# Performance work log

Measured on AMD Instinct MI355X. Metric: run time of the kernel, lower is better.

The kernel has to match this reference:

```python
import jax, jax.numpy as jnp
import numpy as np

TOP_K = 2


def setup_inputs() -> dict:
    key = jax.random.key(0)
    ks = jax.random.split(key, 5)
    B, S, H, E, I = 2, 1024, 1024, 16, 1024
    scale = 1.0 / np.sqrt(H)
    return {
        "hidden_states": jax.random.normal(ks[0], (B, S, H), dtype=jnp.float32),
        "router_w": jax.random.normal(ks[1], (E, H), dtype=jnp.float32) * scale,   # nn.Linear(H,E).weight
        "gate_w": jax.random.normal(ks[2], (E, I, H), dtype=jnp.float32) * scale,  # per-expert Linear(H,I).weight
        "up_w": jax.random.normal(ks[3], (E, I, H), dtype=jnp.float32) * scale,
        "down_w": jax.random.normal(ks[4], (E, H, I), dtype=jnp.float32) * (1.0 / np.sqrt(I)),
    }


def reference(hidden_states, router_w, gate_w, up_w, down_w):
    orig_shape = hidden_states.shape
    x = hidden_states.reshape(-1, orig_shape[-1])  # [T, H]
    T = x.shape[0]
    E = router_w.shape[0]

    # Router: sigmoid -> top-k -> normalize
    logits = jnp.einsum("th,eh->te", x, router_w)           # [T, E]
    scores = jax.nn.sigmoid(logits)
    weights, indices = jax.lax.top_k(scores, TOP_K)         # [T, K]
    weights = weights / (weights.sum(axis=-1, keepdims=True) + 1e-20)

    # Dense per-token-per-expert combine weight (0 for unrouted pairs) ==
    # exact math of the torch gather/index_add loop.
    w_full = jnp.zeros((T, E), dtype=x.dtype).at[
        jnp.arange(T)[:, None], indices
    ].add(weights)                                          # [T, E]

    # Expert MLPs (SwiGLU) computed for all experts, zero-weighted combine.
    g = jax.nn.silu(jnp.einsum("th,eih->tei", x, gate_w))   # [T, E, I]
    u = jnp.einsum("th,eih->tei", x, up_w)                  # [T, E, I]
    out = jnp.einsum("te,tei,ehi->th", w_full, g * u, down_w)  # [T, H]
    return out.reshape(orig_shape)
```

## Files before the change

### kernel.cpp

```cpp
#include <hip/hip_runtime.h>
#include <stdint.h>

#define T_TOK 2048
#define H_DIM 1024
#define E_NUM 16
#define I_DIM 1024
#define TOTAL_ROWS (2 * T_TOK)
#define CPAD 16

typedef short bf16x8 __attribute__((ext_vector_type(8)));
typedef float f32x4 __attribute__((ext_vector_type(4)));

__device__ __forceinline__ void async_copy16(const void* g, void* l) {
  __builtin_amdgcn_global_load_lds(
      (const __attribute__((address_space(1))) void*)g,
      (__attribute__((address_space(3))) void*)l, 16, 0, 0);
}

__device__ __forceinline__ uint32_t f2bf(float f) {
  uint32_t u = __float_as_uint(f);
  return (u + 0x7FFFu + ((u >> 16) & 1u)) >> 16;
}
__device__ __forceinline__ uint32_t pk2bf(float lo, float hi) {
  return f2bf(lo) | (f2bf(hi) << 16);
}

#define WS_COUNTS 0
#define WS_OFFSETS 2048
#define WS_TOKENS 4096
#define WS_WTS (4096 + 131072)
#define WS_XBF (4096 + 262144)
#define WS_HBUF (WS_XBF + 4194304)
#define WS_GBUF (WS_HBUF + 8388608)
#define WS_UBUF (WS_GBUF + 33554432)
#define WS_DBUF (WS_UBUF + 33554432)
#define WS_NEED (WS_DBUF + 33554432)

__global__ __launch_bounds__(256) void router_prep_kernel(
    const float* __restrict__ x, const float* __restrict__ rw,
    const float* __restrict__ gate, const float* __restrict__ up,
    const float* __restrict__ down, uint16_t* __restrict__ xbf,
    int* __restrict__ counts, int* __restrict__ tokens,
    float* __restrict__ wts, uint16_t* __restrict__ gbuf,
    uint16_t* __restrict__ ubuf, uint16_t* __restrict__ dbuf) {
  const int bid = blockIdx.x;
  const int tid = threadIdx.x;

  if (bid < 512) {
    const int t = bid * 4 + (tid >> 6);
    const int lane = tid & 63;

    float4 xv[4];
    float acc[E_NUM];
#pragma unroll
    for (int e = 0; e < E_NUM; ++e) acc[e] = 0.f;

#pragma unroll
    for (int rep = 0; rep < 4; ++rep) {
      const int h0 = rep * 256 + lane * 4;
      xv[rep] = *(const float4*)(x + (size_t)t * H_DIM + h0);
      uint2 p;
      p.x = pk2bf(xv[rep].x, xv[rep].y);
      p.y = pk2bf(xv[rep].z, xv[rep].w);
      *(uint2*)(xbf + (size_t)t * H_DIM + h0) = p;
    }

#pragma unroll
    for (int e = 0; e < E_NUM; ++e) {
#pragma unroll
      for (int rep = 0; rep < 4; ++rep) {
        const float4 rv =
            *(const float4*)(rw + (size_t)e * H_DIM + rep * 256 + lane * 4);
        acc[e] += xv[rep].x * rv.x + xv[rep].y * rv.y + xv[rep].z * rv.z +
                  xv[rep].w * rv.w;
      }
    }

#pragma unroll
    for (int e = 0; e < E_NUM; ++e) {
      float v = acc[e];
#pragma unroll
      for (int off = 32; off > 0; off >>= 1) v += __shfl_xor(v, off);
      acc[e] = v;
    }

    if (lane < 2) {
      float s[E_NUM];
#pragma unroll
      for (int e = 0; e < E_NUM; ++e) s[e] = 1.f / (1.f + expf(-acc[e]));
      int i1 = 0;
      float v1 = s[0];
#pragma unroll
      for (int e = 1; e < E_NUM; ++e)
        if (s[e] > v1) { v1 = s[e]; i1 = e; }
      int i2 = -1;
      float v2 = -1.f;
#pragma unroll
      for (int e = 0; e < E_NUM; ++e)
        if (e != i1 && s[e] > v2) { v2 = s[e]; i2 = e; }
      const float inv = 1.f / (v1 + v2 + 1e-20f);
      const int pe = (lane == 0) ? i1 : i2;
      const float pw = ((lane == 0) ? v1 : v2) * inv;
      const int slot = atomicAdd(&counts[pe * CPAD], 1);
      tokens[pe * T_TOK + slot] = t;
      wts[pe * T_TOK + slot] = pw;
    }
    return;
  }

  const int tt = bid - 512;
  const int mat = tt >> 12;
  const int r = tt & 4095;
  const int e = r >> 8;
  const int nt = (r >> 4) & 15;
  const int kt = r & 15;
  const float* W = (mat == 0) ? gate : (mat == 1) ? up : down;
  uint16_t* D = (mat == 0) ? gbuf : (mat == 1) ? ubuf : dbuf;
  const float* src = W + ((size_t)e * 1024 + (size_t)nt * 64) * 1024 + kt * 64;
  uint16_t* dst = D + ((size_t)((e * 16 + nt) * 16 + kt)) * 4096;

#pragma unroll
  for (int h = 0; h < 2; ++h) {
    const int c = tid + h * 256;
    const int m = c >> 3;
    const int kq = (c & 7) ^ (m & 7);
    const float* s = src + (size_t)m * 1024 + kq * 8;
    const float4 a = *(const float4*)s;
    const float4 b = *(const float4*)(s + 4);
    uint4 p;
    p.x = pk2bf(a.x, a.y);
    p.y = pk2bf(a.z, a.w);
    p.z = pk2bf(b.x, b.y);
    p.w = pk2bf(b.z, b.w);
    *(uint4*)(dst + (size_t)c * 8) = p;
  }
}

__global__ void offsets_kernel(const int* __restrict__ counts,
                               int* __restrict__ offsets) {
  if (threadIdx.x == 0) {
    int a = 0;
    for (int e = 0; e < E_NUM; ++e) {
      offsets[e] = a;
      a += counts[e * CPAD];
    }
    offsets[E_NUM] = a;
  }
}

__global__ __launch_bounds__(256, 2) void gemm1_kernel(
    const uint16_t* __restrict__ xbf, const uint16_t* __restrict__ gbuf,
    const uint16_t* __restrict__ ubuf, const int* __restrict__ counts,
    const int* __restrict__ offsets, const int* __restrict__ tokens,
    const float* __restrict__ wts, uint16_t* __restrict__ hbuf) {
  const int e = blockIdx.z;
  const int count = counts[e * CPAD];
  const int m0 = blockIdx.y * 128;
  if (m0 >= count) return;
  const int n0t = blockIdx.x;

  __shared__ __align__(16) uint16_t As[2][128 * 64];
  __shared__ __align__(16) uint16_t Bgs[2][64 * 64];
  __shared__ __align__(16) uint16_t Bus[2][64 * 64];
  __shared__ int tok_s[128];
  __shared__ float wt_s[128];

  const int tid = threadIdx.x;
  if (tid < 128) {
    const int slot = m0 + tid;
    int tk = 0;
    float w = 0.f;
    if (slot < count) {
      tk = tokens[e * T_TOK + slot];
      w = wts[e * T_TOK + slot];
    }
    tok_s[tid] = tk;
    wt_s[tid] = w;
  }
  __syncthreads();

  const uint16_t* a_g[4];
  int a_c[4];
#pragma unroll
  for (int j = 0; j < 4; ++j) {
    const int c = j * 256 + tid;
    const int m = c >> 3;
    const int kq = (c & 7) ^ (m & 7);
    a_g[j] = xbf + (size_t)tok_s[m] * H_DIM + kq * 8;
    a_c[j] = c * 8;
  }
  const uint16_t* g_g = gbuf + (size_t)((e * 16 + n0t) * 16) * 4096;
  const uint16_t* u_g = ubuf + (size_t)((e * 16 + n0t) * 16) * 4096;
  const int bc0 = tid * 8, bc1 = (tid + 256) * 8;

  const int wave = tid >> 6, lane = tid & 63;
  const int wm = wave * 32;
  const int lc = lane & 15, lq = lane >> 4;
  const int l7 = lc & 7;

  f32x4 accg[2][4], accu[2][4];
  const f32x4 zero4 = {0.f, 0.f, 0.f, 0.f};
#pragma unroll
  for (int i = 0; i < 2; ++i)
#pragma unroll
    for (int j = 0; j < 4; ++j) {
      accg[i][j] = zero4;
      accu[i][j] = zero4;
    }

  int am[2], bn[4];
#pragma unroll
  for (int i = 0; i < 2; ++i) am[i] = (wm + i * 16 + lc) * 64;
#pragma unroll
  for (int i = 0; i < 4; ++i) bn[i] = (i * 16 + lc) * 64;

#pragma unroll
  for (int j = 0; j < 4; ++j) async_copy16(a_g[j], &As[0][a_c[j]]);
  async_copy16(g_g + bc0, &Bgs[0][bc0]);
  async_copy16(g_g + bc1, &Bgs[0][bc1]);
  async_copy16(u_g + bc0, &Bus[0][bc0]);
  async_copy16(u_g + bc1, &Bus[0][bc1]);
  __syncthreads();

  int cur = 0;
  for (int kt = 0; kt < 16; ++kt) {
    const bool more = (kt < 15);
    if (more) {
      const int ko = (kt + 1) * 64;
      const int bo = (kt + 1) * 4096;
      const int nb = cur ^ 1;
#pragma unroll
      for (int j = 0; j < 4; ++j) async_copy16(a_g[j] + ko, &As[nb][a_c[j]]);
      async_copy16(g_g + bo + bc0, &Bgs[nb][bc0]);
      async_copy16(g_g + bo + bc1, &Bgs[nb][bc1]);
      async_copy16(u_g + bo + bc0, &Bus[nb][bc0]);
      async_copy16(u_g + bo + bc1, &Bus[nb][bc1]);
    }

#pragma unroll
    for (int ks = 0; ks < 2; ++ks) {
      const int kswz = ((ks * 4 + lq) ^ l7) * 8;
      bf16x8 af[2], bg[4], bu[4];
#pragma unroll
      for (int i = 0; i < 2; ++i)
        af[i] = *(const bf16x8*)&As[cur][am[i] + kswz];
#pragma unroll
      for (int i = 0; i < 4; ++i) {
        bg[i] = *(const bf16x8*)&Bgs[cur][bn[i] + kswz];
        bu[i] = *(const bf16x8*)&Bus[cur][bn[i] + kswz];
      }
#pragma unroll
      for (int im = 0; im < 2; ++im)
#pragma unroll
        for (int in = 0; in < 4; ++in) {
          accg[im][in] = __builtin_amdgcn_mfma_f32_16x16x32_bf16(
              af[im], bg[in], accg[im][in], 0, 0, 0);
          accu[im][in] = __builtin_amdgcn_mfma_f32_16x16x32_bf16(
              af[im], bu[in], accu[im][in], 0, 0, 0);
        }
    }

    if (more) {
      __syncthreads();
      cur ^= 1;
    }
  }

  const int off_e = offsets[e];
#pragma unroll
  for (int im = 0; im < 2; ++im) {
#pragma unroll
    for (int r = 0; r < 4; ++r) {
      const int row = wm + im * 16 + lq * 4 + r;
      const int slot = m0 + row;
      if (slot < count) {
        const float w = wt_s[row];
        uint16_t* hrow = hbuf + (size_t)(off_e + slot) * I_DIM + n0t * 64;
#pragma unroll
        for (int in = 0; in < 4; ++in) {
          const float g = accg[im][in][r];
          const float u = accu[im][in][r];
          const float hv = g / (1.f + __expf(-g)) * u * w;
          hrow[in * 16 + lc] = (uint16_t)f2bf(hv);
        }
      }
    }
  }
}

__global__ __launch_bounds__(256, 3) void gemm2_kernel(
    const uint16_t* __restrict__ hbuf, const uint16_t* __restrict__ dbuf,
    const int* __restrict__ counts, const int* __restrict__ offsets,
    const int* __restrict__ tokens, float* __restrict__ out) {
  const int e = blockIdx.z;
  const int count = counts[e * CPAD];
  const int m0 = blockIdx.y * 128;
  if (m0 >= count) return;
  const int n0t = blockIdx.x;

  __shared__ __align__(16) uint16_t As[2][128 * 64];
  __shared__ __align__(16) uint16_t Bs[2][64 * 64];
  __shared__ int tok_s[128];

  const int tid = threadIdx.x;
  const int off_e = offsets[e];
  if (tid < 128) {
    const int slot = m0 + tid;
    tok_s[tid] = (slot < count) ? tokens[e * T_TOK + slot] : 0;
  }

  const uint16_t* a_g[4];
  int a_c[4];
#pragma unroll
  for (int j = 0; j < 4; ++j) {
    const int c = j * 256 + tid;
    const int m = c >> 3;
    const int kq = (c & 7) ^ (m & 7);
    int r = off_e + m0 + m;
    if (r > TOTAL_ROWS - 1) r = TOTAL_ROWS - 1;
    a_g[j] = hbuf + (size_t)r * I_DIM + kq * 8;
    a_c[j] = c * 8;
  }
  const uint16_t* d_g = dbuf + (size_t)((e * 16 + n0t) * 16) * 4096;
  const int bc0 = tid * 8, bc1 = (tid + 256) * 8;

  const int wave = tid >> 6, lane = tid & 63;
  const int wm = wave * 32;
  const int lc = lane & 15, lq = lane >> 4;
  const int l7 = lc & 7;

  f32x4 acc[2][4];
  const f32x4 zero4 = {0.f, 0.f, 0.f, 0.f};
#pragma unroll
  for (int i = 0; i < 2; ++i)
#pragma unroll
    for (int j = 0; j < 4; ++j) acc[i][j] = zero4;

  int am[2], bn[4];
#pragma unroll
  for (int i = 0; i < 2; ++i) am[i] = (wm + i * 16 + lc) * 64;
#pragma unroll
  for (int i = 0; i < 4; ++i) bn[i] = (i * 16 + lc) * 64;

  __syncthreads();

#pragma unroll
  for (int j = 0; j < 4; ++j) async_copy16(a_g[j], &As[0][a_c[j]]);
  async_copy16(d_g + bc0, &Bs[0][bc0]);
  async_copy16(d_g + bc1, &Bs[0][bc1]);
  __syncthreads();

  int cur = 0;
  for (int kt = 0; kt < 16; ++kt) {
    const bool more = (kt < 15);
    if (more) {
      const int ko = (kt + 1) * 64;
      const int bo = (kt + 1) * 4096;
      const int nb = cur ^ 1;
#pragma unroll
      for (int j = 0; j < 4; ++j) async_copy16(a_g[j] + ko, &As[nb][a_c[j]]);
      async_copy16(d_g + bo + bc0, &Bs[nb][bc0]);
      async_copy16(d_g + bo + bc1, &Bs[nb][bc1]);
    }

#pragma unroll
    for (int ks = 0; ks < 2; ++ks) {
      const int kswz = ((ks * 4 + lq) ^ l7) * 8;
      bf16x8 af[2], bf[4];
#pragma unroll
      for (int i = 0; i < 2; ++i)
        af[i] = *(const bf16x8*)&As[cur][am[i] + kswz];
#pragma unroll
      for (int i = 0; i < 4; ++i)
        bf[i] = *(const bf16x8*)&Bs[cur][bn[i] + kswz];
#pragma unroll
      for (int im = 0; im < 2; ++im)
#pragma unroll
        for (int in = 0; in < 4; ++in)
          acc[im][in] = __builtin_amdgcn_mfma_f32_16x16x32_bf16(
              af[im], bf[in], acc[im][in], 0, 0, 0);
    }

    if (more) {
      __syncthreads();
      cur ^= 1;
    }
  }

#pragma unroll
  for (int im = 0; im < 2; ++im) {
#pragma unroll
    for (int r = 0; r < 4; ++r) {
      const int row = wm + im * 16 + lq * 4 + r;
      const int slot = m0 + row;
      if (slot < count) {
        float* orow = out + (size_t)tok_s[row] * H_DIM + n0t * 64;
#pragma unroll
        for (int in = 0; in < 4; ++in)
          atomicAdd(orow + in * 16 + lc, acc[im][in][r]);
      }
    }
  }
}

__global__ __launch_bounds__(256, 3) void gemm1_fb(
    const uint16_t* __restrict__ xbf, const float* __restrict__ gate,
    const float* __restrict__ up, const int* __restrict__ counts,
    const int* __restrict__ offsets, const int* __restrict__ tokens,
    const float* __restrict__ wts, uint16_t* __restrict__ hbuf) {
  const int e = blockIdx.z;
  const int count = counts[e * CPAD];
  const int m0 = blockIdx.y * 128;
  if (m0 >= count) return;
  const int n0 = blockIdx.x * 32;

  __shared__ __align__(16) uint16_t As[2][128 * 64];
  __shared__ __align__(16) uint16_t Bgs[2][32 * 64];
  __shared__ __align__(16) uint16_t Bus[2][32 * 64];
  __shared__ int tok_s[128];
  __shared__ float wt_s[128];

  const int tid = threadIdx.x;
  if (tid < 128) {
    const int slot = m0 + tid;
    int tk = 0;
    float w = 0.f;
    if (slot < count) {
      tk = tokens[e * T_TOK + slot];
      w = wts[e * T_TOK + slot];
    }
    tok_s[tid] = tk;
    wt_s[tid] = w;
  }
  __syncthreads();

  const uint16_t* a_g[4];
  int a_c[4];
#pragma unroll
  for (int j = 0; j < 4; ++j) {
    const int c = j * 256 + tid;
    const int m = c >> 3;
    const int kq = (c & 7) ^ (m & 7);
    a_g[j] = xbf + (size_t)tok_s[m] * H_DIM + kq * 8;
    a_c[j] = c * 8;
  }
  const int bm = tid >> 3;
  const int bkq = (tid & 7) ^ (bm & 7);
  const float* g_g = gate + ((size_t)e * I_DIM + n0 + bm) * H_DIM + bkq * 8;
  const float* u_g = up + ((size_t)e * I_DIM + n0 + bm) * H_DIM + bkq * 8;
  const int b_c = tid * 8;

  const int wave = tid >> 6, lane = tid & 63;
  const int wm = wave * 32;
  const int lc = lane & 15, lq = lane >> 4;
  const int l7 = lc & 7;

  f32x4 accg[2][2], accu[2][2];
  const f32x4 zero4 = {0.f, 0.f, 0.f, 0.f};
#pragma unroll
  for (int i = 0; i < 2; ++i)
#pragma unroll
    for (int j = 0; j < 2; ++j) {
      accg[i][j] = zero4;
      accu[i][j] = zero4;
    }

  int am[2], bn[2];
#pragma unroll
  for (int i = 0; i < 2; ++i) am[i] = (wm + i * 16 + lc) * 64;
#pragma unroll
  for (int i = 0; i < 2; ++i) bn[i] = (i * 16 + lc) * 64;

#pragma unroll
  for (int j = 0; j < 4; ++j) async_copy16(a_g[j], &As[0][a_c[j]]);
  float4 g0 = *(const float4*)g_g;
  float4 g1 = *(const float4*)(g_g + 4);
  float4 u0 = *(const float4*)u_g;
  float4 u1 = *(const float4*)(u_g + 4);
  {
    uint4 p;
    p.x = pk2bf(g0.x, g0.y);
    p.y = pk2bf(g0.z, g0.w);
    p.z = pk2bf(g1.x, g1.y);
    p.w = pk2bf(g1.z, g1.w);
    *(uint4*)&Bgs[0][b_c] = p;
    p.x = pk2bf(u0.x, u0.y);
    p.y = pk2bf(u0.z, u0.w);
    p.z = pk2bf(u1.x, u1.y);
    p.w = pk2bf(u1.z, u1.w);
    *(uint4*)&Bus[0][b_c] = p;
  }
  __syncthreads();

  int cur = 0;
  for (int k0 = 0; k0 < H_DIM; k0 += 64) {
    const int nxt = k0 + 64;
    const bool more = (nxt < H_DIM);
    if (more) {
#pragma unroll
      for (int j = 0; j < 4; ++j)
        async_copy16(a_g[j] + nxt, &As[cur ^ 1][a_c[j]]);
      g0 = *(const float4*)(g_g + nxt);
      g1 = *(const float4*)(g_g + nxt + 4);
      u0 = *(const float4*)(u_g + nxt);
      u1 = *(const float4*)(u_g + nxt + 4);
    }

#pragma unroll
    for (int ks = 0; ks < 2; ++ks) {
      const int kswz = ((ks * 4 + lq) ^ l7) * 8;
      bf16x8 af[2], bg[2], bu[2];
#pragma unroll
      for (int i = 0; i < 2; ++i)
        af[i] = *(const bf16x8*)&As[cur][am[i] + kswz];
#pragma unroll
      for (int i = 0; i < 2; ++i) {
        bg[i] = *(const bf16x8*)&Bgs[cur][bn[i] + kswz];
        bu[i] = *(const bf16x8*)&Bus[cur][bn[i] + kswz];
      }
#pragma unroll
      for (int im = 0; im < 2; ++im)
#pragma unroll
        for (int in = 0; in < 2; ++in) {
          accg[im][in] = __builtin_amdgcn_mfma_f32_16x16x32_bf16(
              af[im], bg[in], accg[im][in], 0, 0, 0);
          accu[im][in] = __builtin_amdgcn_mfma_f32_16x16x32_bf16(
              af[im], bu[in], accu[im][in], 0, 0, 0);
        }
    }

    if (more) {
      uint4 p;
      p.x = pk2bf(g0.x, g0.y);
      p.y = pk2bf(g0.z, g0.w);
      p.z = pk2bf(g1.x, g1.y);
      p.w = pk2bf(g1.z, g1.w);
      *(uint4*)&Bgs[cur ^ 1][b_c] = p;
      p.x = pk2bf(u0.x, u0.y);
      p.y = pk2bf(u0.z, u0.w);
      p.z = pk2bf(u1.x, u1.y);
      p.w = pk2bf(u1.z, u1.w);
      *(uint4*)&Bus[cur ^ 1][b_c] = p;
      __syncthreads();
      cur ^= 1;
    }
  }

  const int off_e = offsets[e];
#pragma unroll
  for (int im = 0; im < 2; ++im) {
#pragma unroll
    for (int r = 0; r < 4; ++r) {
      const int row = wm + im * 16 + lq * 4 + r;
      const int slot = m0 + row;
      if (slot < count) {
        const float w = wt_s[row];
        uint16_t* hrow = hbuf + (size_t)(off_e + slot) * I_DIM + n0;
#pragma unroll
        for (int in = 0; in < 2; ++in) {
          const float g = accg[im][in][r];
          const float u = accu[im][in][r];
          const float hv = g / (1.f + __expf(-g)) * u * w;
          hrow[in * 16 + lc] = (uint16_t)f2bf(hv);
        }
      }
    }
  }
}

__global__ __launch_bounds__(256, 3) void gemm2_fb(
    const uint16_t* __restrict__ hbuf, const float* __restrict__ down,
    const int* __restrict__ counts, const int* __restrict__ offsets,
    const int* __restrict__ tokens, float* __restrict__ out) {
  const int e = blockIdx.z;
  const int count = counts[e * CPAD];
  const int m0 = blockIdx.y * 128;
  if (m0 >= count) return;
  const int n0 = blockIdx.x * 32;

  __shared__ __align__(16) uint16_t As[2][128 * 64];
  __shared__ __align__(16) uint16_t Bs[2][32 * 64];
  __shared__ int tok_s[128];

  const int tid = threadIdx.x;
  const int off_e = offsets[e];
  if (tid < 128) {
    const int slot = m0 + tid;
    tok_s[tid] = (slot < count) ? tokens[e * T_TOK + slot] : 0;
  }

  const uint16_t* a_g[4];
  int a_c[4];
#pragma unroll
  for (int j = 0; j < 4; ++j) {
    const int c = j * 256 + tid;
    const int m = c >> 3;
    const int kq = (c & 7) ^ (m & 7);
    int r = off_e + m0 + m;
    if (r > TOTAL_ROWS - 1) r = TOTAL_ROWS - 1;
    a_g[j] = hbuf + (size_t)r * I_DIM + kq * 8;
    a_c[j] = c * 8;
  }
  const int bm = tid >> 3;
  const int bkq = (tid & 7) ^ (bm & 7);
  const float* d_g = down + ((size_t)e * H_DIM + n0 + bm) * I_DIM + bkq * 8;
  const int b_c = tid * 8;

  const int wave = tid >> 6, lane = tid & 63;
  const int wm = wave * 32;
  const int lc = lane & 15, lq = lane >> 4;
  const int l7 = lc & 7;

  f32x4 acc[2][2];
  const f32x4 zero4 = {0.f, 0.f, 0.f, 0.f};
#pragma unroll
  for (int i = 0; i < 2; ++i)
#pragma unroll
    for (int j = 0; j < 2; ++j) acc[i][j] = zero4;

  int am[2], bn[2];
#pragma unroll
  for (int i = 0; i < 2; ++i) am[i] = (wm + i * 16 + lc) * 64;
#pragma unroll
  for (int i = 0; i < 2; ++i) bn[i] = (i * 16 + lc) * 64;

#pragma unroll
  for (int j = 0; j < 4; ++j) async_copy16(a_g[j], &As[0][a_c[j]]);
  float4 d0 = *(const float4*)d_g;
  float4 d1 = *(const float4*)(d_g + 4);
  {
    uint4 p;
    p.x = pk2bf(d0.x, d0.y);
    p.y = pk2bf(d0.z, d0.w);
    p.z = pk2bf(d1.x, d1.y);
    p.w = pk2bf(d1.z, d1.w);
    *(uint4*)&Bs[0][b_c] = p;
  }
  __syncthreads();

  int cur = 0;
  for (int k0 = 0; k0 < I_DIM; k0 += 64) {
    const int nxt = k0 + 64;
    const bool more = (nxt < I_DIM);
    if (more) {
#pragma unroll
      for (int j = 0; j < 4; ++j)
        async_copy16(a_g[j] + nxt, &As[cur ^ 1][a_c[j]]);
      d0 = *(const float4*)(d_g + nxt);
      d1 = *(const float4*)(d_g + nxt + 4);
    }

#pragma unroll
    for (int ks = 0; ks < 2; ++ks) {
      const int kswz = ((ks * 4 + lq) ^ l7) * 8;
      bf16x8 af[2], bf[2];
#pragma unroll
      for (int i = 0; i < 2; ++i)
        af[i] = *(const bf16x8*)&As[cur][am[i] + kswz];
#pragma unroll
      for (int i = 0; i < 2; ++i)
        bf[i] = *(const bf16x8*)&Bs[cur][bn[i] + kswz];
#pragma unroll
      for (int im = 0; im < 2; ++im)
#pragma unroll
        for (int in = 0; in < 2; ++in)
          acc[im][in] = __builtin_amdgcn_mfma_f32_16x16x32_bf16(
              af[im], bf[in], acc[im][in], 0, 0, 0);
    }

    if (more) {
      uint4 p;
      p.x = pk2bf(d0.x, d0.y);
      p.y = pk2bf(d0.z, d0.w);
      p.z = pk2bf(d1.x, d1.y);
      p.w = pk2bf(d1.z, d1.w);
      *(uint4*)&Bs[cur ^ 1][b_c] = p;
      __syncthreads();
      cur ^= 1;
    }
  }

#pragma unroll
  for (int im = 0; im < 2; ++im) {
#pragma unroll
    for (int r = 0; r < 4; ++r) {
      const int row = wm + im * 16 + lq * 4 + r;
      const int slot = m0 + row;
      if (slot < count) {
        float* orow = out + (size_t)tok_s[row] * H_DIM + n0;
#pragma unroll
        for (int in = 0; in < 2; ++in)
          atomicAdd(orow + in * 16 + lc, acc[im][in][r]);
      }
    }
  }
}

extern "C" void kernel_launch(void* const* d_in, const int* in_sizes, int n_in,
                              void* d_out, int out_size, void* d_ws,
                              size_t ws_size, hipStream_t stream) {
  const float* x = (const float*)d_in[0];
  const float* rw = (const float*)d_in[1];
  const float* gate = (const float*)d_in[2];
  const float* up = (const float*)d_in[3];
  const float* down = (const float*)d_in[4];
  float* out = (float*)d_out;

  uint8_t* ws = (uint8_t*)d_ws;
  int* counts = (int*)(ws + WS_COUNTS);
  int* offsets = (int*)(ws + WS_OFFSETS);
  int* tokens = (int*)(ws + WS_TOKENS);
  float* wts = (float*)(ws + WS_WTS);
  uint16_t* xbf = (uint16_t*)(ws + WS_XBF);
  uint16_t* hbuf = (uint16_t*)(ws + WS_HBUF);
  uint16_t* gbuf = (uint16_t*)(ws + WS_GBUF);
  uint16_t* ubuf = (uint16_t*)(ws + WS_UBUF);
  uint16_t* dbuf = (uint16_t*)(ws + WS_DBUF);

  const bool big = (ws_size >= (size_t)WS_NEED);

  hipMemsetAsync(counts, 0, 2048, stream);
  hipMemsetAsync(out, 0, (size_t)out_size * sizeof(float), stream);

  if (big) {
    router_prep_kernel<<<512 + 12288, 256, 0, stream>>>(
        x, rw, gate, up, down, xbf, counts, tokens, wts, gbuf, ubuf, dbuf);
    offsets_kernel<<<1, 64, 0, stream>>>(counts, offsets);
    gemm1_kernel<<<dim3(16, 16, 16), 256, 0, stream>>>(
        xbf, gbuf, ubuf, counts, offsets, tokens, wts, hbuf);
    gemm2_kernel<<<dim3(16, 16, 16), 256, 0, stream>>>(hbuf, dbuf, counts,
                                                       offsets, tokens, out);
  } else {
    router_prep_kernel<<<512, 256, 0, stream>>>(
        x, rw, gate, up, down, xbf, counts, tokens, wts, gbuf, ubuf, dbuf);
    offsets_kernel<<<1, 64, 0, stream>>>(counts, offsets);
    gemm1_fb<<<dim3(32, 16, 16), 256, 0, stream>>>(
        xbf, gate, up, counts, offsets, tokens, wts, hbuf);
    gemm2_fb<<<dim3(32, 16, 16), 256, 0, stream>>>(hbuf, down, counts,
                                                   offsets, tokens, out);
  }
}
```

Baseline: 303.6 us.

## Use partial vmcnt waits so next-stage loads overlap MFMA compute in grouped GEMMs

Restructures the double-buffered K loops of both expert GEMM kernels. Before, each iteration ended with a full __syncthreads, which drains all outstanding global-to-LDS copies, including the prefetch for the next tile. Now the loop issues the next stage's async copies, waits only for the older stage with s_waitcnt vmcnt(N), and uses raw s_barrier plus sched_barrier fences, so the prefetch stays in flight during the MFMA work. The weight-conversion kernel is also manually unrolled so both loads are issued before the packing. The hand-counted vmcnt values must match the exact number of copies per stage, and miscounting would cause races.

```diff
diff --git a/kernel.cpp b/kernel.cpp
--- a/kernel.cpp
+++ b/kernel.cpp
@@ -119,21 +119,27 @@
   const float* src = W + ((size_t)e * 1024 + (size_t)nt * 64) * 1024 + kt * 64;
   uint16_t* dst = D + ((size_t)((e * 16 + nt) * 16 + kt)) * 4096;
 
-#pragma unroll
-  for (int h = 0; h < 2; ++h) {
-    const int c = tid + h * 256;
-    const int m = c >> 3;
-    const int kq = (c & 7) ^ (m & 7);
-    const float* s = src + (size_t)m * 1024 + kq * 8;
-    const float4 a = *(const float4*)s;
-    const float4 b = *(const float4*)(s + 4);
-    uint4 p;
-    p.x = pk2bf(a.x, a.y);
-    p.y = pk2bf(a.z, a.w);
-    p.z = pk2bf(b.x, b.y);
-    p.w = pk2bf(b.z, b.w);
-    *(uint4*)(dst + (size_t)c * 8) = p;
-  }
+  const int c0 = tid;
+  const int m0c = c0 >> 3, kq0 = (c0 & 7) ^ (m0c & 7);
+  const int c1 = tid + 256;
+  const int m1c = c1 >> 3, kq1 = (c1 & 7) ^ (m1c & 7);
+  const float* s0 = src + (size_t)m0c * 1024 + kq0 * 8;
+  const float* s1 = src + (size_t)m1c * 1024 + kq1 * 8;
+  const float4 a0 = *(const float4*)s0;
+  const float4 b0 = *(const float4*)(s0 + 4);
+  const float4 a1 = *(const float4*)s1;
+  const float4 b1 = *(const float4*)(s1 + 4);
+  uint4 p0, p1;
+  p0.x = pk2bf(a0.x, a0.y);
+  p0.y = pk2bf(a0.z, a0.w);
+  p0.z = pk2bf(b0.x, b0.y);
+  p0.w = pk2bf(b0.z, b0.w);
+  p1.x = pk2bf(a1.x, a1.y);
+  p1.y = pk2bf(a1.z, a1.w);
+  p1.z = pk2bf(b1.x, b1.y);
+  p1.w = pk2bf(b1.z, b1.w);
+  *(uint4*)(dst + (size_t)c0 * 8) = p0;
+  *(uint4*)(dst + (size_t)c1 * 8) = p1;
 }
 
 __global__ void offsets_kernel(const int* __restrict__ counts,
@@ -147,6 +153,15 @@
     offsets[E_NUM] = a;
   }
 }
+
+#define WAIT_VM(N)                                         \
+  asm volatile("s_waitcnt vmcnt(" #N ")" ::: "memory");    \
+  __builtin_amdgcn_s_barrier();                            \
+  __builtin_amdgcn_sched_barrier(0);
+
+#define TAIL_BAR()                                         \
+  __builtin_amdgcn_sched_barrier(0);                       \
+  __builtin_amdgcn_s_barrier();
 
 __global__ __launch_bounds__(256, 2) void gemm1_kernel(
     const uint16_t* __restrict__ xbf, const uint16_t* __restrict__ gbuf,
@@ -214,57 +229,48 @@
 #pragma unroll
   for (int i = 0; i < 4; ++i) bn[i] = (i * 16 + lc) * 64;
 
-#pragma unroll
-  for (int j = 0; j < 4; ++j) async_copy16(a_g[j], &As[0][a_c[j]]);
-  async_copy16(g_g + bc0, &Bgs[0][bc0]);
-  async_copy16(g_g + bc1, &Bgs[0][bc1]);
-  async_copy16(u_g + bc0, &Bus[0][bc0]);
-  async_copy16(u_g + bc1, &Bus[0][bc1]);
-  __syncthreads();
-
+#define G1_STAGE(BUF, KT)                                                 \
+  {                                                                       \
+    const int ko_ = (KT)*64;                                              \
+    const int bo_ = (KT)*4096;                                            \
+    _Pragma("unroll") for (int j = 0; j < 4; ++j)                         \
+        async_copy16(a_g[j] + ko_, &As[BUF][a_c[j]]);                     \
+    async_copy16(g_g + bo_ + bc0, &Bgs[BUF][bc0]);                        \
+    async_copy16(g_g + bo_ + bc1, &Bgs[BUF][bc1]);                        \
+    async_copy16(u_g + bo_ + bc0, &Bus[BUF][bc0]);                        \
+    async_copy16(u_g + bo_ + bc1, &Bus[BUF][bc1]);                        \
+  }
+
+#define G1_COMPUTE(CB)                                                    \
+  _Pragma("unroll") for (int ks = 0; ks < 2; ++ks) {                      \
+    const int kswz = ((ks * 4 + lq) ^ l7) * 8;                            \
+    bf16x8 af[2], bg[4], bu[4];                                           \
+    _Pragma("unroll") for (int i = 0; i < 2; ++i) af[i] =                 \
+        *(const bf16x8*)&As[CB][am[i] + kswz];                            \
+    _Pragma("unroll") for (int i = 0; i < 4; ++i) {                       \
+      bg[i] = *(const bf16x8*)&Bgs[CB][bn[i] + kswz];                     \
+      bu[i] = *(const bf16x8*)&Bus[CB][bn[i] + kswz];                     \
+    }                                                                     \
+    _Pragma("unroll") for (int im = 0; im < 2; ++im)                      \
+        _Pragma("unroll") for (int in = 0; in < 4; ++in) {                \
+      accg[im][in] = __builtin_amdgcn_mfma_f32_16x16x32_bf16(             \
+          af[im], bg[in], accg[im][in], 0, 0, 0);                         \
+      accu[im][in] = __builtin_amdgcn_mfma_f32_16x16x32_bf16(             \
+          af[im], bu[in], accu[im][in], 0, 0, 0);                         \
+    }                                                                     \
+  }
+
+  G1_STAGE(0, 0)
   int cur = 0;
-  for (int kt = 0; kt < 16; ++kt) {
-    const bool more = (kt < 15);
-    if (more) {
-      const int ko = (kt + 1) * 64;
-      const int bo = (kt + 1) * 4096;
-      const int nb = cur ^ 1;
-#pragma unroll
-      for (int j = 0; j < 4; ++j) async_copy16(a_g[j] + ko, &As[nb][a_c[j]]);
-      async_copy16(g_g + bo + bc0, &Bgs[nb][bc0]);
-      async_copy16(g_g + bo + bc1, &Bgs[nb][bc1]);
-      async_copy16(u_g + bo + bc0, &Bus[nb][bc0]);
-      async_copy16(u_g + bo + bc1, &Bus[nb][bc1]);
-    }
-
-#pragma unroll
-    for (int ks = 0; ks < 2; ++ks) {
-      const int kswz = ((ks * 4 + lq) ^ l7) * 8;
-      bf16x8 af[2], bg[4], bu[4];
-#pragma unroll
-      for (int i = 0; i < 2; ++i)
-        af[i] = *(const bf16x8*)&As[cur][am[i] + kswz];
-#pragma unroll
-      for (int i = 0; i < 4; ++i) {
-        bg[i] = *(const bf16x8*)&Bgs[cur][bn[i] + kswz];
-        bu[i] = *(const bf16x8*)&Bus[cur][bn[i] + kswz];
-      }
-#pragma unroll
-      for (int im = 0; im < 2; ++im)
-#pragma unroll
-        for (int in = 0; in < 4; ++in) {
-          accg[im][in] = __builtin_amdgcn_mfma_f32_16x16x32_bf16(
-              af[im], bg[in], accg[im][in], 0, 0, 0);
-          accu[im][in] = __builtin_amdgcn_mfma_f32_16x16x32_bf16(
-              af[im], bu[in], accu[im][in], 0, 0, 0);
-        }
-    }
-
-    if (more) {
-      __syncthreads();
-      cur ^= 1;
-    }
-  }
+  for (int kt = 0; kt < 15; ++kt) {
+    G1_STAGE(cur ^ 1, kt + 1)
+    WAIT_VM(8)
+    G1_COMPUTE(cur)
+    TAIL_BAR()
+    cur ^= 1;
+  }
+  WAIT_VM(0)
+  G1_COMPUTE(cur)
 
   const int off_e = offsets[e];
 #pragma unroll
@@ -344,48 +350,41 @@
 
   __syncthreads();
 
-#pragma unroll
-  for (int j = 0; j < 4; ++j) async_copy16(a_g[j], &As[0][a_c[j]]);
-  async_copy16(d_g + bc0, &Bs[0][bc0]);
-  async_copy16(d_g + bc1, &Bs[0][bc1]);
-  __syncthreads();
-
+#define G2_STAGE(BUF, KT)                                                 \
+  {                                                                       \
+    const int ko_ = (KT)*64;                                              \
+    const int bo_ = (KT)*4096;                                            \
+    _Pragma("unroll") for (int j = 0; j < 4; ++j)                         \
+        async_copy16(a_g[j] + ko_, &As[BUF][a_c[j]]);                     \
+    async_copy16(d_g + bo_ + bc0, &Bs[BUF][bc0]);                         \
+    async_copy16(d_g + bo_ + bc1, &Bs[BUF][bc1]);                         \
+  }
+
+#define G2_COMPUTE(CB)                                                    \
+  _Pragma("unroll") for (int ks = 0; ks < 2; ++ks) {                      \
+    const int kswz = ((ks * 4 + lq) ^ l7) * 8;                            \
+    bf16x8 af[2], bf[4];                                                  \
+    _Pragma("unroll") for (int i = 0; i < 2; ++i) af[i] =                 \
+        *(const bf16x8*)&As[CB][am[i] + kswz];                            \
+    _Pragma("unroll") for (int i = 0; i < 4; ++i) bf[i] =                 \
+        *(const bf16x8*)&Bs[CB][bn[i] + kswz];                            \
+    _Pragma("unroll") for (int im = 0; im < 2; ++im)                      \
+        _Pragma("unroll") for (int in = 0; in < 4; ++in) acc[im][in] =    \
+            __builtin_amdgcn_mfma_f32_16x16x32_bf16(af[im], bf[in],       \
+                                                    acc[im][in], 0, 0, 0);\
+  }
+
+  G2_STAGE(0, 0)
   int cur = 0;
-  for (int kt = 0; kt < 16; ++kt) {
-    const bool more = (kt < 15);
-    if (more) {
-      const int ko = (kt + 1) * 64;
-      const int bo = (kt + 1) * 4096;
-      const int nb = cur ^ 1;
-#pragma unroll
-      for (int j = 0; j < 4; ++j) async_copy16(a_g[j] + ko, &As[nb][a_c[j]]);
-      async_copy16(d_g + bo + bc0, &Bs[nb][bc0]);
-      async_copy16(d_g + bo + bc1, &Bs[nb][bc1]);
-    }
-
-#pragma unroll
-    for (int ks = 0; ks < 2; ++ks) {
-      const int kswz = ((ks * 4 + lq) ^ l7) * 8;
-      bf16x8 af[2], bf[4];
-#pragma unroll
-      for (int i = 0; i < 2; ++i)
-        af[i] = *(const bf16x8*)&As[cur][am[i] + kswz];
-#pragma unroll
-      for (int i = 0; i < 4; ++i)
-        bf[i] = *(const bf16x8*)&Bs[cur][bn[i] + kswz];
-#pragma unroll
-      for (int im = 0; im < 2; ++im)
-#pragma unroll
-        for (int in = 0; in < 4; ++in)
-          acc[im][in] = __builtin_amdgcn_mfma_f32_16x16x32_bf16(
-              af[im], bf[in], acc[im][in], 0, 0, 0);
-    }
-
-    if (more) {
-      __syncthreads();
-      cur ^= 1;
-    }
-  }
+  for (int kt = 0; kt < 15; ++kt) {
+    G2_STAGE(cur ^ 1, kt + 1)
+    WAIT_VM(6)
+    G2_COMPUTE(cur)
+    TAIL_BAR()
+    cur ^= 1;
+  }
+  WAIT_VM(0)
+  G2_COMPUTE(cur)
 
 #pragma unroll
   for (int im = 0; im < 2; ++im) {
```

After: 292.3 us. 1.04x faster.
